# Optimization experiments

Hardware: AMD Instinct MI355X
Metric: run time of the kernel (lower is better)

## Reference

```python
import jax, jax.numpy as jnp
import numpy as np

TOP_K = 2  # cfg.MODEL.MOE.TOP_K


def setup_inputs() -> dict:
    key = jax.random.key(0)
    ks = jax.random.split(key, 5)
    bs, L, d_in, d_out, E = 32, 1024, 768, 256, 8
    return {
        "x": jax.random.normal(ks[0], (bs, L, d_in), dtype=jnp.float32),
        "gate_W": jax.random.normal(ks[1], (d_in, E), dtype=jnp.float32) * (1.0 / np.sqrt(d_in)),
        "gate_b": jax.random.normal(ks[2], (E,), dtype=jnp.float32) * 0.01,
        "expert_W": jax.random.normal(ks[3], (E, d_in, d_out), dtype=jnp.float32) * (1.0 / np.sqrt(d_in)),
        "expert_b": jax.random.normal(ks[4], (E, d_out), dtype=jnp.float32) * 0.01,
    }


def reference(x, gate_W, gate_b, expert_W, expert_b):
    # Gate: (bs, L, E) softmax over experts, then top-k routing weights.
    gate_logits = jnp.einsum("bli,ie->ble", x, gate_W) + gate_b
    gate_weights = jax.nn.softmax(gate_logits, axis=-1)
    topk_vals, topk_idx = jax.lax.top_k(gate_weights, TOP_K)  # (bs, L, K)

    # Dense all-expert projection (E is small), then gather the selected ones.
    # all_out: (bs, L, E, d_out)
    all_out = jnp.einsum("bli,eio->bleo", x, expert_W) + expert_b

    # Select top-k expert outputs per token: (bs, L, K, d_out)
    sel = jnp.take_along_axis(all_out, topk_idx[..., None], axis=2)

    # Weighted combine over the K routed experts -> (bs, L, d_out)
    output = jnp.sum(sel * topk_vals[..., None], axis=2)
    return output
```

## Files before the change

### kernel.cpp

```cpp
#include <hip/hip_runtime.h>
#include <hip/hip_bf16.h>
#include <stdint.h>

#define T_TOKENS 32768
#define D_IN     768
#define D_OUT    256
#define N_EXP    8
#define S_TOT    (T_TOKENS*2)
#define S_PAD    66560
#define KSPLIT   6
#define NKB      24

typedef __attribute__((ext_vector_type(8))) short bf16x8;
typedef __attribute__((ext_vector_type(4))) float f32x4;

__device__ __forceinline__ unsigned short f2bf(float f) {
    unsigned u = __float_as_uint(f);
    return (unsigned short)((u + 0x7FFFu + ((u >> 16) & 1u)) >> 16);
}
__device__ __forceinline__ unsigned pack_bf2(float a, float b) {
    return (unsigned)f2bf(a) | ((unsigned)f2bf(b) << 16);
}

__device__ __forceinline__ void async16(void* lds, const void* g) {
    __builtin_amdgcn_global_load_lds(
        (const __attribute__((address_space(1))) unsigned int*)g,
        (__attribute__((address_space(3))) unsigned int*)lds, 16, 0, 0);
}

__global__ __launch_bounds__(256) void convw_kernel(
        const float* __restrict__ W, unsigned short* __restrict__ WTb,
        int* __restrict__ zero16) {
    if (blockIdx.x == 0 && threadIdx.x < 16) zero16[threadIdx.x] = 0;
    int eb_ = blockIdx.x;
    int n = threadIdx.x;
    const float* src = W + ((size_t)(eb_ / NKB) * D_IN + (eb_ % NKB) * 32) * 256 + n;
    unsigned pk[16];
    #pragma unroll
    for (int j = 0; j < 16; j++)
        pk[j] = pack_bf2(src[(2*j) * 256], src[(2*j+1) * 256]);
    unsigned* dst = (unsigned*)(WTb + ((size_t)eb_ * 256 + n) * 32);
    #pragma unroll
    for (int j = 0; j < 16; j++) dst[j] = pk[j];
}

__global__ __launch_bounds__(64) void gate_partial_kernel(
        const float* __restrict__ x, const float* __restrict__ gW,
        unsigned short* __restrict__ xbf, float* __restrict__ partial) {
    __shared__ float tile[64 * 65];
    int tid = threadIdx.x;
    int t0  = blockIdx.x * 64;
    int kq  = blockIdx.y;
    int c16 = tid & 15, rb = tid >> 4;
    float acc[8] = {0,0,0,0,0,0,0,0};
    #pragma unroll 1
    for (int j = 0; j < 2; j++) {
        int kc = kq * 128 + j * 64;
        #pragma unroll
        for (int i = 0; i < 16; i++) {
            int row = i * 4 + rb;
            size_t g = (size_t)(t0 + row) * D_IN + kc + c16 * 4;
            float4 v = *(const float4*)(x + g);
            uint2 p; p.x = pack_bf2(v.x, v.y); p.y = pack_bf2(v.z, v.w);
            *(uint2*)(xbf + g) = p;
            float* d = &tile[row * 65 + c16 * 4];
            d[0] = v.x; d[1] = v.y; d[2] = v.z; d[3] = v.w;
        }
        __syncthreads();
        const float* gr = gW + (size_t)kc * 8;
        #pragma unroll 8
        for (int kk = 0; kk < 64; kk++) {
            float xv = tile[tid * 65 + kk];
            #pragma unroll
            for (int e = 0; e < 8; e++) acc[e] += xv * gr[kk * 8 + e];
        }
        __syncthreads();
    }
    float* dst = partial + ((size_t)kq * T_TOKENS + t0 + tid) * 8;
    float4 o0 = {acc[0], acc[1], acc[2], acc[3]};
    float4 o1 = {acc[4], acc[5], acc[6], acc[7]};
    *(float4*)dst = o0; *(float4*)(dst + 4) = o1;
}

__global__ __launch_bounds__(256) void gate_final_kernel(
        const float* __restrict__ partial, const float* __restrict__ gb,
        float* __restrict__ topk_w, int* __restrict__ topk_e, int* __restrict__ counts) {
    __shared__ int h[8];
    int tid = threadIdx.x;
    if (tid < 8) h[tid] = 0;
    __syncthreads();
    int t = blockIdx.x * 256 + tid;
    float acc[8] = {0,0,0,0,0,0,0,0};
    #pragma unroll
    for (int q = 0; q < KSPLIT; q++) {
        const float* p = partial + ((size_t)q * T_TOKENS + t) * 8;
        float4 a = *(const float4*)p;
        float4 b = *(const float4*)(p + 4);
        acc[0] += a.x; acc[1] += a.y; acc[2] += a.z; acc[3] += a.w;
        acc[4] += b.x; acc[5] += b.y; acc[6] += b.z; acc[7] += b.w;
    }
    float mx = -1e30f;
    #pragma unroll
    for (int e = 0; e < 8; e++) { acc[e] += gb[e]; mx = fmaxf(mx, acc[e]); }
    float w[8], s = 0.f;
    #pragma unroll
    for (int e = 0; e < 8; e++) { w[e] = expf(acc[e] - mx); s += w[e]; }
    float inv = 1.0f / s;
    int e0 = 0; float b0 = -1.f;
    #pragma unroll
    for (int e = 0; e < 8; e++) if (w[e] > b0) { b0 = w[e]; e0 = e; }
    int e1 = 0; float b1 = -1.f;
    #pragma unroll
    for (int e = 0; e < 8; e++) if (e != e0 && w[e] > b1) { b1 = w[e]; e1 = e; }
    topk_w[t*2]   = b0 * inv;
    topk_w[t*2+1] = b1 * inv;
    topk_e[t*2]   = e0;
    topk_e[t*2+1] = e1;
    atomicAdd(&h[e0], 1); atomicAdd(&h[e1], 1);
    __syncthreads();
    if (tid < 8) atomicAdd(&counts[tid], h[tid]);
}

__global__ void scatter_kernel(const int* __restrict__ topk_e, const float* __restrict__ topk_w,
                               const int* __restrict__ counts, int* __restrict__ cursors,
                               int* __restrict__ slot_token, float* __restrict__ slot_w,
                               int* __restrict__ inv_slot) {
    int offs[9]; offs[0] = 0;
    #pragma unroll
    for (int e = 0; e < 8; e++) offs[e+1] = offs[e] + ((counts[e] + 127) & ~127);
    __shared__ int hcnt[8], hbase[8];
    if (threadIdx.x < 8) hcnt[threadIdx.x] = 0;
    __syncthreads();
    int idx[4], ee[4], lr[4];
    int base = blockIdx.x * 256 * 4 + threadIdx.x;
    #pragma unroll
    for (int j = 0; j < 4; j++) {
        idx[j] = base + j * 256;
        ee[j]  = topk_e[idx[j]];
        lr[j]  = atomicAdd(&hcnt[ee[j]], 1);
    }
    __syncthreads();
    if (threadIdx.x < 8) hbase[threadIdx.x] = atomicAdd(&cursors[threadIdx.x], hcnt[threadIdx.x]);
    __syncthreads();
    #pragma unroll
    for (int j = 0; j < 4; j++) {
        int slot = offs[ee[j]] + hbase[ee[j]] + lr[j];
        slot_token[slot] = idx[j] >> 1;
        slot_w[slot]     = topk_w[idx[j]];
        inv_slot[idx[j]] = slot;
    }
}

template<bool ROUTED>
__global__ __launch_bounds__(512, 4) void moe_gemm_kernel(
        const unsigned short* __restrict__ xbf, const unsigned short* __restrict__ WTb,
        const float* __restrict__ eb, const int* __restrict__ counts,
        const int* __restrict__ slot_token, const float* __restrict__ slot_w,
        float* __restrict__ dst) {
    __shared__ unsigned short A_lds[3][128 * 32];
    __shared__ unsigned short B_lds[3][256 * 32];

    int lbid = (blockIdx.x & 7) * ((int)gridDim.x >> 3) + (blockIdx.x >> 3);

    int offs[9]; offs[0] = 0;
    #pragma unroll
    for (int e = 0; e < 8; e++) offs[e+1] = offs[e] + ((counts[e] + 127) & ~127);
    int row0 = lbid * 128;
    if (row0 >= offs[8]) return;
    int expert = 0;
    #pragma unroll
    for (int e = 0; e < 8; e++) if (row0 >= offs[e]) expert = e;

    int tid  = threadIdx.x;
    int wave = tid >> 6, lane = tid & 63;
    int lrow = lane & 15, lquad = lane >> 4;
    int wm = wave >> 2, wn = wave & 3;

    int ar = tid >> 2, ap = tid & 3;
    int alc = (ap - (ar >> 1)) & 3;
    int tok = slot_token[row0 + ar];
    tok = (tok < 0 || tok >= T_TOKENS) ? 0 : tok;
    const unsigned short* asrc = xbf + (size_t)tok * D_IN + alc * 8;

    const unsigned short* bexp = WTb + (size_t)expert * NKB * 8192;
    int boff[2];
    #pragma unroll
    for (int i = 0; i < 2; i++) {
        int c = i * 512 + tid;
        int r = c >> 2, p = c & 3;
        int lc = (p - (r >> 1)) & 3;
        boff[i] = r * 32 + lc * 8;
    }

    int a_off[4], b_off[4];
    #pragma unroll
    for (int m = 0; m < 4; m++) {
        int r = wm * 64 + m * 16 + lrow;
        a_off[m] = r * 32 + ((lquad + (r >> 1)) & 3) * 8;
    }
    #pragma unroll
    for (int q = 0; q < 4; q++) {
        int r = wn * 64 + q * 16 + lrow;
        b_off[q] = r * 32 + ((lquad + (r >> 1)) & 3) * 8;
    }

    f32x4 acc[4][4];
    #pragma unroll
    for (int m = 0; m < 4; m++)
        #pragma unroll
        for (int q = 0; q < 4; q++) acc[m][q] = (f32x4){0,0,0,0};

    auto stage = [&](int kb, int st) {
        async16(&A_lds[st][tid * 8], asrc + kb * 32);
        const unsigned short* tb = bexp + (size_t)kb * 8192;
        #pragma unroll
        for (int i = 0; i < 2; i++)
            async16(&B_lds[st][(i * 512 + tid) * 8], tb + boff[i]);
    };

    stage(0, 0);
    stage(1, 1);
    for (int s = 0; s < NKB; s++) {
        if (s == NKB - 1) asm volatile("s_waitcnt vmcnt(0)" ::: "memory");
        else              asm volatile("s_waitcnt vmcnt(3)" ::: "memory");
        asm volatile("s_barrier" ::: "memory");
        if (s + 2 < NKB) stage(s + 2, (s + 2) % 3);
        int p = s % 3;
        bf16x8 a[4], b[4];
        #pragma unroll
        for (int m = 0; m < 4; m++) a[m] = *(const bf16x8*)&A_lds[p][a_off[m]];
        #pragma unroll
        for (int q = 0; q < 4; q++) b[q] = *(const bf16x8*)&B_lds[p][b_off[q]];
        __builtin_amdgcn_s_setprio(1);
        #pragma unroll
        for (int q = 0; q < 4; q++)
            #pragma unroll
            for (int m = 0; m < 4; m++)
                acc[m][q] = __builtin_amdgcn_mfma_f32_16x16x32_bf16(a[m], b[q], acc[m][q], 0, 0, 0);
        __builtin_amdgcn_s_setprio(0);
    }

    float bias_q[4];
    #pragma unroll
    for (int q = 0; q < 4; q++) bias_q[q] = eb[expert * D_OUT + wn * 64 + q * 16 + lrow];
    #pragma unroll
    for (int m = 0; m < 4; m++) {
        #pragma unroll
        for (int r = 0; r < 4; r++) {
            int slot = row0 + wm * 64 + m * 16 + lquad * 4 + r;
            if constexpr (ROUTED) {
                float* drow = dst + (size_t)slot * D_OUT + wn * 64;
                #pragma unroll
                for (int q = 0; q < 4; q++)
                    drow[q * 16 + lrow] = acc[m][q][r] + bias_q[q];
            } else {
                int tk = slot_token[slot];
                float wgt = slot_w[slot];
                #pragma unroll
                for (int q = 0; q < 4; q++)
                    atomicAdd(dst + (size_t)tk * D_OUT + wn * 64 + q * 16 + lrow,
                              wgt * (acc[m][q][r] + bias_q[q]));
            }
        }
    }
}

__global__ void combine_kernel(const float* __restrict__ routed, const int* __restrict__ inv_slot,
                               const float* __restrict__ topk_w, float* __restrict__ out) {
    int flat = blockIdx.x * 256 + threadIdx.x;
    int t = flat >> 6, c = (flat & 63) * 4;
    int   s0 = inv_slot[t*2], s1 = inv_slot[t*2+1];
    float w0 = topk_w[t*2],   w1 = topk_w[t*2+1];
    float4 r0 = *(const float4*)(routed + (size_t)s0 * D_OUT + c);
    float4 r1 = *(const float4*)(routed + (size_t)s1 * D_OUT + c);
    float4 o;
    o.x = w0*r0.x + w1*r1.x; o.y = w0*r0.y + w1*r1.y;
    o.z = w0*r0.z + w1*r1.z; o.w = w0*r0.w + w1*r1.w;
    *(float4*)(out + (size_t)t * D_OUT + c) = o;
}

extern "C" void kernel_launch(void* const* d_in, const int* in_sizes, int n_in,
                              void* d_out, int out_size, void* d_ws, size_t ws_size,
                              hipStream_t stream) {
    const float* x  = (const float*)d_in[0];
    const float* gW = (const float*)d_in[1];
    const float* gb = (const float*)d_in[2];
    const float* eW = (const float*)d_in[3];
    const float* eb = (const float*)d_in[4];
    float* out = (float*)d_out;
    char* ws = (char*)d_ws;

    float* topk_w      = (float*)(ws + 0);
    int*   topk_e      = (int*)  (ws + 262144);
    int*   counts      = (int*)  (ws + 524288);
    int*   cursors     = (int*)  (ws + 524320);
    int*   slot_token  = (int*)  (ws + 524416);
    float* slot_w      = (float*)(ws + 790656);
    int*   inv_slot    = (int*)  (ws + 1056896);
    float* partial     = (float*)(ws + 1319040);
    unsigned short* WTb= (unsigned short*)(ws + 7610496);
    unsigned short* xbf= (unsigned short*)(ws + 10756224);
    float* routed      = (float*)(ws + 61087872);
    const size_t NEED_ROUTED = 61087872 + (size_t)S_PAD * D_OUT * 4;
    bool use_routed = (ws_size >= NEED_ROUTED);

    convw_kernel       <<<N_EXP * NKB, 256, 0, stream>>>(eW, WTb, counts);
    gate_partial_kernel<<<dim3(T_TOKENS / 64, KSPLIT), 64, 0, stream>>>(x, gW, xbf, partial);
    gate_final_kernel  <<<T_TOKENS / 256, 256, 0, stream>>>(partial, gb, topk_w, topk_e, counts);
    scatter_kernel     <<<S_TOT / (256 * 4), 256, 0, stream>>>(topk_e, topk_w, counts, cursors,
                                                               slot_token, slot_w, inv_slot);
    if (use_routed) {
        moe_gemm_kernel<true><<<S_PAD / 128, 512, 0, stream>>>(xbf, WTb, eb, counts,
                                                               slot_token, slot_w, routed);
        combine_kernel<<<T_TOKENS * D_OUT / 4 / 256, 256, 0, stream>>>(routed, inv_slot,
                                                                       topk_w, out);
    } else {
        hipMemsetAsync(slot_token, 0, 532480, stream);
        hipMemsetAsync(out, 0, (size_t)out_size * sizeof(float), stream);
        moe_gemm_kernel<false><<<S_PAD / 128, 512, 0, stream>>>(xbf, WTb, eb, counts,
                                                                slot_token, slot_w, out);
    }
}
```

Measured before the change: 257.4 us.

## Fuse weighted combine into MoE GEMM epilogue via atomics and split output columns

Removes the routed intermediate buffer and the separate combine kernel, so the GEMM epilogue scatters weighted results straight into the zeroed output with float atomicAdd. The GEMM now uses 256-thread blocks, each covering 128 rows by 128 output columns, with twice as many blocks, which halves the B tile and doubles the A loads per block. This avoids writing and re-reading a large fp32 intermediate, but adds atomic contention, two memsets, and reloads each gathered activation tile once per column half. Padded slots are skipped through a zero-weight check.

```diff
diff --git a/kernel.cpp b/kernel.cpp
--- a/kernel.cpp
+++ b/kernel.cpp
@@ -123,8 +123,7 @@
 
 __global__ void scatter_kernel(const int* __restrict__ topk_e, const float* __restrict__ topk_w,
                                const int* __restrict__ counts, int* __restrict__ cursors,
-                               int* __restrict__ slot_token, float* __restrict__ slot_w,
-                               int* __restrict__ inv_slot) {
+                               int* __restrict__ slot_token, float* __restrict__ slot_w) {
     int offs[9]; offs[0] = 0;
     #pragma unroll
     for (int e = 0; e < 8; e++) offs[e+1] = offs[e] + ((counts[e] + 127) & ~127);
@@ -147,25 +146,25 @@
         int slot = offs[ee[j]] + hbase[ee[j]] + lr[j];
         slot_token[slot] = idx[j] >> 1;
         slot_w[slot]     = topk_w[idx[j]];
-        inv_slot[idx[j]] = slot;
-    }
-}
-
-template<bool ROUTED>
-__global__ __launch_bounds__(512, 4) void moe_gemm_kernel(
+    }
+}
+
+__global__ __launch_bounds__(256, 3) void moe_gemm_kernel(
         const unsigned short* __restrict__ xbf, const unsigned short* __restrict__ WTb,
         const float* __restrict__ eb, const int* __restrict__ counts,
         const int* __restrict__ slot_token, const float* __restrict__ slot_w,
-        float* __restrict__ dst) {
+        float* __restrict__ out) {
     __shared__ unsigned short A_lds[3][128 * 32];
-    __shared__ unsigned short B_lds[3][256 * 32];
+    __shared__ unsigned short B_lds[3][128 * 32];
 
     int lbid = (blockIdx.x & 7) * ((int)gridDim.x >> 3) + (blockIdx.x >> 3);
+    int ch   = lbid & 1;
+    int trow = lbid >> 1;
 
     int offs[9]; offs[0] = 0;
     #pragma unroll
     for (int e = 0; e < 8; e++) offs[e+1] = offs[e] + ((counts[e] + 127) & ~127);
-    int row0 = lbid * 128;
+    int row0 = trow * 128;
     if (row0 >= offs[8]) return;
     int expert = 0;
     #pragma unroll
@@ -174,19 +173,23 @@
     int tid  = threadIdx.x;
     int wave = tid >> 6, lane = tid & 63;
     int lrow = lane & 15, lquad = lane >> 4;
-    int wm = wave >> 2, wn = wave & 3;
-
-    int ar = tid >> 2, ap = tid & 3;
-    int alc = (ap - (ar >> 1)) & 3;
-    int tok = slot_token[row0 + ar];
-    tok = (tok < 0 || tok >= T_TOKENS) ? 0 : tok;
-    const unsigned short* asrc = xbf + (size_t)tok * D_IN + alc * 8;
-
-    const unsigned short* bexp = WTb + (size_t)expert * NKB * 8192;
+    int wm = wave >> 1, wn = wave & 1;
+
+    const unsigned short* asrc[2];
+    #pragma unroll
+    for (int i = 0; i < 2; i++) {
+        int c = i * 256 + tid;
+        int r = c >> 2, p = c & 3;
+        int lc = (p - (r >> 1)) & 3;
+        int tok = slot_token[row0 + r];
+        tok = (tok < 0 || tok >= T_TOKENS) ? 0 : tok;
+        asrc[i] = xbf + (size_t)tok * D_IN + lc * 8;
+    }
+    const unsigned short* bexp = WTb + (size_t)expert * NKB * 8192 + ch * 4096;
     int boff[2];
     #pragma unroll
     for (int i = 0; i < 2; i++) {
-        int c = i * 512 + tid;
+        int c = i * 256 + tid;
         int r = c >> 2, p = c & 3;
         int lc = (p - (r >> 1)) & 3;
         boff[i] = r * 32 + lc * 8;
@@ -211,18 +214,20 @@
         for (int q = 0; q < 4; q++) acc[m][q] = (f32x4){0,0,0,0};
 
     auto stage = [&](int kb, int st) {
-        async16(&A_lds[st][tid * 8], asrc + kb * 32);
+        #pragma unroll
+        for (int i = 0; i < 2; i++)
+            async16(&A_lds[st][(i * 256 + tid) * 8], asrc[i] + kb * 32);
         const unsigned short* tb = bexp + (size_t)kb * 8192;
         #pragma unroll
         for (int i = 0; i < 2; i++)
-            async16(&B_lds[st][(i * 512 + tid) * 8], tb + boff[i]);
+            async16(&B_lds[st][(i * 256 + tid) * 8], tb + boff[i]);
     };
 
     stage(0, 0);
     stage(1, 1);
     for (int s = 0; s < NKB; s++) {
         if (s == NKB - 1) asm volatile("s_waitcnt vmcnt(0)" ::: "memory");
-        else              asm volatile("s_waitcnt vmcnt(3)" ::: "memory");
+        else              asm volatile("s_waitcnt vmcnt(4)" ::: "memory");
         asm volatile("s_barrier" ::: "memory");
         if (s + 2 < NKB) stage(s + 2, (s + 2) % 3);
         int p = s % 3;
@@ -242,41 +247,23 @@
 
     float bias_q[4];
     #pragma unroll
-    for (int q = 0; q < 4; q++) bias_q[q] = eb[expert * D_OUT + wn * 64 + q * 16 + lrow];
+    for (int q = 0; q < 4; q++)
+        bias_q[q] = eb[expert * D_OUT + ch * 128 + wn * 64 + q * 16 + lrow];
     #pragma unroll
     for (int m = 0; m < 4; m++) {
         #pragma unroll
         for (int r = 0; r < 4; r++) {
             int slot = row0 + wm * 64 + m * 16 + lquad * 4 + r;
-            if constexpr (ROUTED) {
-                float* drow = dst + (size_t)slot * D_OUT + wn * 64;
+            int tk   = slot_token[slot];
+            float wgt = slot_w[slot];
+            if (wgt != 0.f) {
+                float* drow = out + (size_t)tk * D_OUT + ch * 128 + wn * 64;
                 #pragma unroll
                 for (int q = 0; q < 4; q++)
-                    drow[q * 16 + lrow] = acc[m][q][r] + bias_q[q];
-            } else {
-                int tk = slot_token[slot];
-                float wgt = slot_w[slot];
-                #pragma unroll
-                for (int q = 0; q < 4; q++)
-                    atomicAdd(dst + (size_t)tk * D_OUT + wn * 64 + q * 16 + lrow,
-                              wgt * (acc[m][q][r] + bias_q[q]));
+                    atomicAdd(drow + q * 16 + lrow, wgt * (acc[m][q][r] + bias_q[q]));
             }
         }
     }
-}
-
-__global__ void combine_kernel(const float* __restrict__ routed, const int* __restrict__ inv_slot,
-                               const float* __restrict__ topk_w, float* __restrict__ out) {
-    int flat = blockIdx.x * 256 + threadIdx.x;
-    int t = flat >> 6, c = (flat & 63) * 4;
-    int   s0 = inv_slot[t*2], s1 = inv_slot[t*2+1];
-    float w0 = topk_w[t*2],   w1 = topk_w[t*2+1];
-    float4 r0 = *(const float4*)(routed + (size_t)s0 * D_OUT + c);
-    float4 r1 = *(const float4*)(routed + (size_t)s1 * D_OUT + c);
-    float4 o;
-    o.x = w0*r0.x + w1*r1.x; o.y = w0*r0.y + w1*r1.y;
-    o.z = w0*r0.z + w1*r1.z; o.w = w0*r0.w + w1*r1.w;
-    *(float4*)(out + (size_t)t * D_OUT + c) = o;
 }
 
 extern "C" void kernel_launch(void* const* d_in, const int* in_sizes, int n_in,
@@ -296,28 +283,18 @@
     int*   cursors     = (int*)  (ws + 524320);
     int*   slot_token  = (int*)  (ws + 524416);
     float* slot_w      = (float*)(ws + 790656);
-    int*   inv_slot    = (int*)  (ws + 1056896);
     float* partial     = (float*)(ws + 1319040);
     unsigned short* WTb= (unsigned short*)(ws + 7610496);
     unsigned short* xbf= (unsigned short*)(ws + 10756224);
-    float* routed      = (float*)(ws + 61087872);
-    const size_t NEED_ROUTED = 61087872 + (size_t)S_PAD * D_OUT * 4;
-    bool use_routed = (ws_size >= NEED_ROUTED);
+
+    hipMemsetAsync(slot_token, 0, 532480, stream);
+    hipMemsetAsync(out, 0, (size_t)out_size * sizeof(float), stream);
 
     convw_kernel       <<<N_EXP * NKB, 256, 0, stream>>>(eW, WTb, counts);
     gate_partial_kernel<<<dim3(T_TOKENS / 64, KSPLIT), 64, 0, stream>>>(x, gW, xbf, partial);
     gate_final_kernel  <<<T_TOKENS / 256, 256, 0, stream>>>(partial, gb, topk_w, topk_e, counts);
     scatter_kernel     <<<S_TOT / (256 * 4), 256, 0, stream>>>(topk_e, topk_w, counts, cursors,
-                                                               slot_token, slot_w, inv_slot);
-    if (use_routed) {
-        moe_gemm_kernel<true><<<S_PAD / 128, 512, 0, stream>>>(xbf, WTb, eb, counts,
-                                                               slot_token, slot_w, routed);
-        combine_kernel<<<T_TOKENS * D_OUT / 4 / 256, 256, 0, stream>>>(routed, inv_slot,
-                                                                       topk_w, out);
-    } else {
-        hipMemsetAsync(slot_token, 0, 532480, stream);
-        hipMemsetAsync(out, 0, (size_t)out_size * sizeof(float), stream);
-        moe_gemm_kernel<false><<<S_PAD / 128, 512, 0, stream>>>(xbf, WTb, eb, counts,
-                                                                slot_token, slot_w, out);
-    }
-}
+                                                               slot_token, slot_w);
+    moe_gemm_kernel<<<(S_PAD / 128) * 2, 256, 0, stream>>>(xbf, WTb, eb, counts,
+                                                           slot_token, slot_w, out);
+}
```

Result: slower. 281.1 us (+9.2%).

## Load expert weights directly from global into registers, drop B LDS staging

Applied to the files above, without the earlier changes.

The GEMM kernel stops staging the expert weight tile through shared memory. Each wave now loads its B fragments straight from global memory into double-buffered registers one k-step ahead, and only the gathered A rows still go through async LDS copies, with the vmcnt wait adjusted to match. The scatter kernel also zeroes slot weights in the padding rows so the non-routed path can skip atomics for padded slots. This cuts LDS traffic and footprint, which may allow more occupancy, but it relies on the weight layout being usable directly as fragments and gives up the sharing of B loads across waves.

```diff
diff --git a/kernel.cpp b/kernel.cpp
--- a/kernel.cpp
+++ b/kernel.cpp
@@ -128,6 +128,13 @@
     int offs[9]; offs[0] = 0;
     #pragma unroll
     for (int e = 0; e < 8; e++) offs[e+1] = offs[e] + ((counts[e] + 127) & ~127);
+    if (blockIdx.x == 0) {
+        #pragma unroll
+        for (int e = 0; e < 8; e++) {
+            int start = offs[e] + counts[e];
+            for (int i = start + threadIdx.x; i < offs[e+1]; i += 256) slot_w[i] = 0.f;
+        }
+    }
     __shared__ int hcnt[8], hbase[8];
     if (threadIdx.x < 8) hcnt[threadIdx.x] = 0;
     __syncthreads();
@@ -158,7 +165,6 @@
         const int* __restrict__ slot_token, const float* __restrict__ slot_w,
         float* __restrict__ dst) {
     __shared__ unsigned short A_lds[3][128 * 32];
-    __shared__ unsigned short B_lds[3][256 * 32];
 
     int lbid = (blockIdx.x & 7) * ((int)gridDim.x >> 3) + (blockIdx.x >> 3);
 
@@ -182,27 +188,15 @@
     tok = (tok < 0 || tok >= T_TOKENS) ? 0 : tok;
     const unsigned short* asrc = xbf + (size_t)tok * D_IN + alc * 8;
 
-    const unsigned short* bexp = WTb + (size_t)expert * NKB * 8192;
-    int boff[2];
-    #pragma unroll
-    for (int i = 0; i < 2; i++) {
-        int c = i * 512 + tid;
-        int r = c >> 2, p = c & 3;
-        int lc = (p - (r >> 1)) & 3;
-        boff[i] = r * 32 + lc * 8;
-    }
-
-    int a_off[4], b_off[4];
+    const unsigned short* bptr = WTb + (size_t)expert * NKB * 8192
+                                     + (wn * 64 + lrow) * 32 + lquad * 8;
+
+    int a_off[4];
     #pragma unroll
     for (int m = 0; m < 4; m++) {
         int r = wm * 64 + m * 16 + lrow;
         a_off[m] = r * 32 + ((lquad + (r >> 1)) & 3) * 8;
     }
-    #pragma unroll
-    for (int q = 0; q < 4; q++) {
-        int r = wn * 64 + q * 16 + lrow;
-        b_off[q] = r * 32 + ((lquad + (r >> 1)) & 3) * 8;
-    }
 
     f32x4 acc[4][4];
     #pragma unroll
@@ -210,39 +204,46 @@
         #pragma unroll
         for (int q = 0; q < 4; q++) acc[m][q] = (f32x4){0,0,0,0};
 
-    auto stage = [&](int kb, int st) {
-        async16(&A_lds[st][tid * 8], asrc + kb * 32);
-        const unsigned short* tb = bexp + (size_t)kb * 8192;
-        #pragma unroll
-        for (int i = 0; i < 2; i++)
-            async16(&B_lds[st][(i * 512 + tid) * 8], tb + boff[i]);
+    bf16x8 bA[4], bB[4];
+    auto bload = [&](int kb, bf16x8 (&b)[4]) {
+        const unsigned short* bp = bptr + (size_t)kb * 8192;
+        #pragma unroll
+        for (int q = 0; q < 4; q++) b[q] = *(const bf16x8*)(bp + q * 512);
     };
 
-    stage(0, 0);
-    stage(1, 1);
-    for (int s = 0; s < NKB; s++) {
+    auto kstep = [&](int s, bf16x8 (&bcur)[4], bf16x8 (&bnxt)[4]) {
         if (s == NKB - 1) asm volatile("s_waitcnt vmcnt(0)" ::: "memory");
-        else              asm volatile("s_waitcnt vmcnt(3)" ::: "memory");
+        else              asm volatile("s_waitcnt vmcnt(5)" ::: "memory");
         asm volatile("s_barrier" ::: "memory");
-        if (s + 2 < NKB) stage(s + 2, (s + 2) % 3);
+        if (s + 1 < NKB) bload(s + 1, bnxt);
+        if (s + 2 < NKB)
+            async16(&A_lds[(s + 2) % 3][tid * 8], asrc + (s + 2) * 32);
         int p = s % 3;
-        bf16x8 a[4], b[4];
+        bf16x8 a[4];
         #pragma unroll
         for (int m = 0; m < 4; m++) a[m] = *(const bf16x8*)&A_lds[p][a_off[m]];
-        #pragma unroll
-        for (int q = 0; q < 4; q++) b[q] = *(const bf16x8*)&B_lds[p][b_off[q]];
         __builtin_amdgcn_s_setprio(1);
         #pragma unroll
         for (int q = 0; q < 4; q++)
             #pragma unroll
             for (int m = 0; m < 4; m++)
-                acc[m][q] = __builtin_amdgcn_mfma_f32_16x16x32_bf16(a[m], b[q], acc[m][q], 0, 0, 0);
+                acc[m][q] = __builtin_amdgcn_mfma_f32_16x16x32_bf16(a[m], bcur[q], acc[m][q], 0, 0, 0);
         __builtin_amdgcn_s_setprio(0);
+    };
+
+    async16(&A_lds[0][tid * 8], asrc);
+    __builtin_amdgcn_sched_barrier(0);
+    bload(0, bA);
+    async16(&A_lds[1][tid * 8], asrc + 32);
+    for (int s = 0; s < NKB; s += 2) {
+        kstep(s, bA, bB);
+        kstep(s + 1, bB, bA);
     }
 
     float bias_q[4];
     #pragma unroll
-    for (int q = 0; q < 4; q++) bias_q[q] = eb[expert * D_OUT + wn * 64 + q * 16 + lrow];
+    for (int q = 0; q < 4; q++)
+        bias_q[q] = eb[expert * D_OUT + wn * 64 + q * 16 + lrow];
     #pragma unroll
     for (int m = 0; m < 4; m++) {
         #pragma unroll
@@ -256,10 +257,12 @@
             } else {
                 int tk = slot_token[slot];
                 float wgt = slot_w[slot];
-                #pragma unroll
-                for (int q = 0; q < 4; q++)
-                    atomicAdd(dst + (size_t)tk * D_OUT + wn * 64 + q * 16 + lrow,
-                              wgt * (acc[m][q][r] + bias_q[q]));
+                if (wgt != 0.f) {
+                    #pragma unroll
+                    for (int q = 0; q < 4; q++)
+                        atomicAdd(dst + (size_t)tk * D_OUT + wn * 64 + q * 16 + lrow,
+                                  wgt * (acc[m][q][r] + bias_q[q]));
+                }
             }
         }
     }
```

After: 262.0 us. No clear change (+1.8%).
